# Kernel tuning notes

Measured on AMD Instinct MI355X. Metric: run time of the kernel, lower is better.

The kernel has to match this reference:

```python
import jax, jax.numpy as jnp
import numpy as np

B, S, D, H = 4096, 200, 128, 64


def setup_inputs() -> dict:
    key = jax.random.key(0)
    ks = jax.random.split(key, 8)
    X_series = jax.random.normal(ks[0], (B, S, D), dtype=jnp.float32)
    pos_series = jax.random.normal(ks[1], (S, D), dtype=jnp.float32)
    X_item = jax.random.normal(ks[2], (B, D), dtype=jnp.float32)
    valid_mask = jax.random.randint(ks[3], (B, S), 0, 2) > 0
    valid_mask = valid_mask.at[:, 0].set(True)  # avoid all-masked rows (NaN softmax)
    glorot = jax.nn.initializers.glorot_uniform()
    Wc = glorot(ks[4], (D, H), jnp.float32)
    Wp = glorot(ks[5], (D, H), jnp.float32)
    We = glorot(ks[6], (D, H), jnp.float32)
    z = jax.random.normal(ks[7], (H,), dtype=jnp.float32) * 0.1
    return {"X_series": X_series, "pos_series": pos_series, "X_item": X_item,
            "valid_mask": valid_mask, "Wc": Wc, "Wp": Wp, "We": We, "z": z}


def reference(X_series, pos_series, X_item, valid_mask, Wc, Wp, We, z):
    # additive attention pre-activation: [B,S,H]
    pre = (X_item @ Wc)[:, None, :] + X_series @ We + (pos_series @ Wp)[None, :, :]
    # scores: sum over hidden of z * tanh(pre) -> [B,S]
    scores = jnp.einsum('bsh,h->bs', jnp.tanh(pre), z)
    # raw masked score sum (pre-softmax), [B,1]
    score_sum = jnp.sum(jnp.where(valid_mask, scores, 0.0), axis=-1, keepdims=True)
    # masked softmax over seq
    attn = jax.nn.softmax(jnp.where(valid_mask, scores, -jnp.inf), axis=-1)
    # weighted sum over seq -> [B,D]
    attention_output = jnp.einsum('bs,bsd->bd', attn, X_series)
    return jnp.concatenate([attention_output, score_sum], axis=1)
```

## Files before the change

kernel.cpp:

```cpp
#include <hip/hip_runtime.h>

#define BB 4096
#define SS 200
#define DD 128
#define HH 64
#define NT 13
#define OUTW (DD + 1)

typedef __attribute__((ext_vector_type(4))) float f32x4;
typedef _Float16 f16x8 __attribute__((ext_vector_type(8)));

template <int CTRL>
__device__ __forceinline__ float dpp_add(float x) {
  int xi = __float_as_int(x);
  int yi = __builtin_amdgcn_update_dpp(xi, xi, CTRL, 0xF, 0xF, false);
  return x + __int_as_float(yi);
}
__device__ __forceinline__ float row16_sum(float x) {
  x = dpp_add<0xB1>(x);
  x = dpp_add<0x4E>(x);
  x = dpp_add<0x124>(x);
  x = dpp_add<0x128>(x);
  return x;
}

__global__ void setup_kernel(const float* __restrict__ pos,
                             const float* __restrict__ Wp,
                             const float* __restrict__ We,
                             const void* __restrict__ maskv,
                             float* __restrict__ Pmat,
                             _Float16* __restrict__ Bfrag,
                             int* __restrict__ flag) {
  __shared__ int anyf[4];
  const int blk = blockIdx.x;
  const int t = threadIdx.x;
  if (blk < SS) {
    if (t < HH) {
      float acc = 0.f;
      #pragma unroll 8
      for (int d = 0; d < DD; ++d) acc = fmaf(pos[blk * DD + d], Wp[d * HH + t], acc);
      Pmat[blk * HH + t] = acc;
    }
  } else if (blk == SS) {
    for (int id = t; id < 1024; id += 256) {
      int lane = id & 63;
      int kt = (id >> 6) & 3;
      int ct = id >> 8;
      int kbase = kt * 32 + 8 * (lane >> 4);
      int n = ct * 16 + (lane & 15);
      _Float16* dst = Bfrag + id * 8;
      #pragma unroll
      for (int j = 0; j < 8; ++j) dst[j] = (_Float16)We[(kbase + j) * HH + n];
    }
  } else {
    const unsigned char* mb = (const unsigned char*)maskv;
    int local = 0;
    for (int i = t; i < 4096; i += 256)
      if ((i & 3) != 0 && mb[i] != 0) local = 1;
    unsigned long long bal = __ballot(local != 0);
    if ((t & 63) == 0) anyf[t >> 6] = (bal != 0ull) ? 1 : 0;
    __syncthreads();
    if (t == 0) *flag = (anyf[0] | anyf[1] | anyf[2] | anyf[3]);
  }
}

__global__ void swizzle_kernel(const float* __restrict__ Pmat, _Float16* __restrict__ Psw) {
  const int tile = blockIdx.x;
  const int tid = threadIdx.x;
  const int half = tid >> 6, lane = tid & 63;
  _Float16* dst = Psw + ((size_t)(tile * 2 + half) * 64 + lane) * 8;
  #pragma unroll
  for (int e = 0; e < 8; ++e) {
    const int ct = (half << 1) | (e >> 2);
    const int r = e & 3;
    int s = tile * 16 + ((lane >> 4) << 2) + r;
    if (s >= SS) s = SS - 1;
    dst[e] = (_Float16)Pmat[s * HH + ct * 16 + (lane & 15)];
  }
}

__global__ __launch_bounds__(512, 2) void fused_kernel(
    const float* __restrict__ Xs, const float* __restrict__ Xi,
    const void* __restrict__ maskv, const float* __restrict__ Wc,
    const float* __restrict__ zv,
    const _Float16* __restrict__ Comb,
    const int* __restrict__ flagp,
    float* __restrict__ out) {
  __shared__ __align__(16) _Float16 bf_lds[8192];
  __shared__ __align__(16) float xlds[8][2][2048];

  const int t = threadIdx.x;
  const int lane = t & 63;
  const int w = t >> 6;
  const int lg = lane >> 4;
  const int lr = lane & 15;
  const int b = blockIdx.x * 8 + w;

  const float* Xrow = Xs + (size_t)b * (SS * DD);
  const f16x8* pswb = (const f16x8*)(Comb + 8192);

  auto stage_tile = [&](int tt, int buf) {
    float* dst = &xlds[w][buf][0];
    #pragma unroll
    for (int k = 0; k < 8; ++k) {
      const int row = 2 * k + (lane >> 5);
      int grow = tt * 16 + row; if (grow >= SS) grow = SS - 1;
      const int c = (lane & 31) ^ row;
      const float* src = Xrow + (size_t)grow * DD + c * 4;
      __builtin_amdgcn_global_load_lds(
          (const __attribute__((address_space(1))) void*)src,
          (__attribute__((address_space(3))) void*)(dst + k * 256),
          16, 0, 0);
    }
  };

  stage_tile(0, 0);
  f16x8 pn0 = pswb[lane];
  f16x8 pn1 = pswb[64 + lane];

  {
    const f32x4* src = (const f32x4*)Comb;
    f32x4* dst = (f32x4*)bf_lds;
    dst[t] = src[t];
    dst[t + 512] = src[t + 512];
  }

  float c = 0.f;
  {
    const float* xi = Xi + (size_t)b * DD;
    const float* wc = Wc + lane;
    #pragma unroll 8
    for (int d = 0; d < DD; ++d) c = fmaf(xi[d], wc[d * HH], c);
  }

  const int mflag = *flagp;
  unsigned mbits = 0;
  if (mflag) {
    const unsigned char* mbp = (const unsigned char*)maskv + (size_t)b * SS;
    #pragma unroll
    for (int tt = 0; tt < NT; ++tt) {
      const int srow = tt * 16 + lr;
      unsigned v = (srow < SS) ? (unsigned)mbp[srow] : 0u;
      mbits |= (v ? 1u : 0u) << tt;
    }
  } else {
    const int* mip = (const int*)maskv + (size_t)b * SS;
    #pragma unroll
    for (int tt = 0; tt < NT; ++tt) {
      const int srow = tt * 16 + lr;
      unsigned v = (srow < SS) ? (unsigned)(mip[srow] != 0) : 0u;
      mbits |= v << tt;
    }
  }

  float c4[4], z4[4];
  {
    const float zl = zv[lane];
    #pragma unroll
    for (int ct = 0; ct < 4; ++ct) {
      c4[ct] = __shfl(c, ct * 16 + lr, 64);
      z4[ct] = __shfl(zl, ct * 16 + lr, 64);
    }
  }
  __syncthreads();

  const f16x8* bp = (const f16x8*)bf_lds;
  float part[4][8];
  #pragma unroll
  for (int kt = 0; kt < 4; ++kt)
    #pragma unroll
    for (int j = 0; j < 8; ++j) part[kt][j] = 0.f;
  float usum = 0.f, ssum = 0.f;
  int cur = 0;

  for (int tt = 0; tt < NT; ++tt) {
    asm volatile("s_waitcnt vmcnt(0)" ::: "memory");
    __builtin_amdgcn_sched_barrier(0);
    f32x4 acc[4];
    #pragma unroll
    for (int ct = 0; ct < 4; ++ct) {
      #pragma unroll
      for (int r = 0; r < 4; ++r) {
        const float pv = (ct < 2) ? (float)pn0[ct * 4 + r] : (float)pn1[(ct - 2) * 4 + r];
        acc[ct][r] = pv + c4[ct];
      }
    }
    if (tt + 1 < NT) {
      stage_tile(tt + 1, cur ^ 1);
      pn0 = pswb[(tt + 1) * 128 + lane];
      pn1 = pswb[(tt + 1) * 128 + 64 + lane];
    }
    const float* bufp = &xlds[w][cur][0];
    f16x8 af[4];
    #pragma unroll
    for (int kt = 0; kt < 4; ++kt) {
      const int ch = lg * 2 + kt * 8;
      const f32x4 v0 = *(const f32x4*)&bufp[lr * 128 + (((ch    ) ^ lr) * 4)];
      const f32x4 v1 = *(const f32x4*)&bufp[lr * 128 + (((ch + 1) ^ lr) * 4)];
      f16x8 v;
      v[0] = (_Float16)v0[0]; v[1] = (_Float16)v0[1];
      v[2] = (_Float16)v0[2]; v[3] = (_Float16)v0[3];
      v[4] = (_Float16)v1[0]; v[5] = (_Float16)v1[1];
      v[6] = (_Float16)v1[2]; v[7] = (_Float16)v1[3];
      af[kt] = v;
    }
    #pragma unroll
    for (int kt = 0; kt < 4; ++kt)
      #pragma unroll
      for (int ct = 0; ct < 4; ++ct)
        acc[ct] = __builtin_amdgcn_mfma_f32_16x16x32_f16(af[kt], bp[(ct * 4 + kt) * 64 + lane],
                                                         acc[ct], 0, 0, 0);
    float sc[4];
    #pragma unroll
    for (int r = 0; r < 4; ++r) {
      float p = 0.f;
      #pragma unroll
      for (int ct = 0; ct < 4; ++ct) {
        const float e2 = __expf(2.f * acc[ct][r]);
        const float th = 1.f - 2.f * __builtin_amdgcn_rcpf(e2 + 1.f);
        p = fmaf(z4[ct], th, p);
      }
      sc[r] = row16_sum(p);
    }
    const float s01 = (lr & 1) ? sc[1] : sc[0];
    const float s23 = (lr & 1) ? sc[3] : sc[2];
    const float sel = (lr & 2) ? s23 : s01;
    const float mysc = __shfl(sel, ((lr >> 2) << 4) | lr, 64);
    const bool mv = (mbits >> tt) & 1u;
    const float u = mv ? __expf(mysc) : 0.f;
    ssum += mv ? mysc : 0.f;
    usum += u;
    #pragma unroll
    for (int kt = 0; kt < 4; ++kt)
      #pragma unroll
      for (int j = 0; j < 8; ++j)
        part[kt][j] = fmaf(u, (float)af[kt][j], part[kt][j]);
    cur ^= 1;
  }

  #pragma unroll
  for (int kt = 0; kt < 4; ++kt)
    #pragma unroll
    for (int j = 0; j < 8; ++j)
      part[kt][j] = row16_sum(part[kt][j]);
  usum = row16_sum(usum);
  ssum = row16_sum(ssum);

  const float inv = 1.f / usum;
  if (lr == 0) {
    float* ob = out + (size_t)b * OUTW;
    #pragma unroll
    for (int kt = 0; kt < 4; ++kt)
      #pragma unroll
      for (int j = 0; j < 8; ++j)
        ob[kt * 32 + lg * 8 + j] = part[kt][j] * inv;
  }
  if (lane == 8) out[(size_t)b * OUTW + DD] = ssum;
}

extern "C" void kernel_launch(void* const* d_in, const int* in_sizes, int n_in,
                              void* d_out, int out_size, void* d_ws, size_t ws_size,
                              hipStream_t stream) {
  const float* Xs  = (const float*)d_in[0];
  const float* pos = (const float*)d_in[1];
  const float* Xi  = (const float*)d_in[2];
  const void*  mk  = d_in[3];
  const float* Wc  = (const float*)d_in[4];
  const float* Wp  = (const float*)d_in[5];
  const float* We  = (const float*)d_in[6];
  const float* zv  = (const float*)d_in[7];
  float* out = (float*)d_out;

  char* ws = (char*)d_ws;
  int*      flag  = (int*)ws;
  float*    Pmat  = (float*)(ws + 256);
  _Float16* Bfrag = (_Float16*)(ws + 256 + SS * HH * 4);
  _Float16* Psw   = (_Float16*)(ws + 256 + SS * HH * 4 + 16384);

  setup_kernel<<<SS + 2, 256, 0, stream>>>(pos, Wp, We, mk, Pmat, Bfrag, flag);
  swizzle_kernel<<<NT, 128, 0, stream>>>(Pmat, Psw);
  fused_kernel<<<BB / 8, 512, 0, stream>>>(Xs, Xi, mk, Wc, zv, Bfrag, flag, out);
}
```

Baseline: 106.5 us.

## Prefetch two tiles ahead and hold MFMA B operands in registers

The X-tile staging pipeline goes from one tile ahead to two tiles ahead. The loop is unrolled by two with a partial vmcnt wait, and each buffer is refilled only after its LDS reads have drained. The combined weight fragments move from shared memory into 16 per-lane registers, which removes the LDS copy, the block barrier and the per-MFMA LDS loads. The cost is higher register pressure under launch_bounds(512,2) and reliance on hand-counted vmcnt values.

```diff
diff --git a/kernel.cpp b/kernel.cpp
--- a/kernel.cpp
+++ b/kernel.cpp
@@ -86,7 +86,6 @@
     const _Float16* __restrict__ Comb,
     const int* __restrict__ flagp,
     float* __restrict__ out) {
-  __shared__ __align__(16) _Float16 bf_lds[8192];
   __shared__ __align__(16) float xlds[8][2][2048];
 
   const int t = threadIdx.x;
@@ -114,15 +113,16 @@
     }
   };
 
+  f16x8 pnA0 = pswb[lane],       pnA1 = pswb[64 + lane];
   stage_tile(0, 0);
-  f16x8 pn0 = pswb[lane];
-  f16x8 pn1 = pswb[64 + lane];
-
+  f16x8 pnB0 = pswb[128 + lane], pnB1 = pswb[192 + lane];
+  stage_tile(1, 1);
+
+  f16x8 bfr[16];
   {
-    const f32x4* src = (const f32x4*)Comb;
-    f32x4* dst = (f32x4*)bf_lds;
-    dst[t] = src[t];
-    dst[t + 512] = src[t + 512];
+    const f16x8* bg = (const f16x8*)Comb;
+    #pragma unroll
+    for (int i = 0; i < 16; ++i) bfr[i] = bg[i * 64 + lane];
   }
 
   float c = 0.f;
@@ -162,54 +162,57 @@
       z4[ct] = __shfl(zl, ct * 16 + lr, 64);
     }
   }
-  __syncthreads();
-
-  const f16x8* bp = (const f16x8*)bf_lds;
+
   float part[4][8];
   #pragma unroll
   for (int kt = 0; kt < 4; ++kt)
     #pragma unroll
     for (int j = 0; j < 8; ++j) part[kt][j] = 0.f;
   float usum = 0.f, ssum = 0.f;
-  int cur = 0;
-
-  for (int tt = 0; tt < NT; ++tt) {
-    asm volatile("s_waitcnt vmcnt(0)" ::: "memory");
+
+  auto body = [&](int tt, f16x8& p0, f16x8& p1, int bufIdx, bool last) {
+    if (last) { asm volatile("s_waitcnt vmcnt(0)" ::: "memory"); }
+    else      { asm volatile("s_waitcnt vmcnt(10)" ::: "memory"); }
     __builtin_amdgcn_sched_barrier(0);
     f32x4 acc[4];
     #pragma unroll
     for (int ct = 0; ct < 4; ++ct) {
       #pragma unroll
       for (int r = 0; r < 4; ++r) {
-        const float pv = (ct < 2) ? (float)pn0[ct * 4 + r] : (float)pn1[(ct - 2) * 4 + r];
+        const float pv = (ct < 2) ? (float)p0[ct * 4 + r] : (float)p1[(ct - 2) * 4 + r];
         acc[ct][r] = pv + c4[ct];
       }
     }
-    if (tt + 1 < NT) {
-      stage_tile(tt + 1, cur ^ 1);
-      pn0 = pswb[(tt + 1) * 128 + lane];
-      pn1 = pswb[(tt + 1) * 128 + 64 + lane];
-    }
-    const float* bufp = &xlds[w][cur][0];
-    f16x8 af[4];
+    const float* bufp = &xlds[w][bufIdx][0];
+    f32x4 v0[4], v1[4];
     #pragma unroll
     for (int kt = 0; kt < 4; ++kt) {
       const int ch = lg * 2 + kt * 8;
-      const f32x4 v0 = *(const f32x4*)&bufp[lr * 128 + (((ch    ) ^ lr) * 4)];
-      const f32x4 v1 = *(const f32x4*)&bufp[lr * 128 + (((ch + 1) ^ lr) * 4)];
+      v0[kt] = *(const f32x4*)&bufp[lr * 128 + (((ch    ) ^ lr) * 4)];
+      v1[kt] = *(const f32x4*)&bufp[lr * 128 + (((ch + 1) ^ lr) * 4)];
+    }
+    asm volatile("s_waitcnt lgkmcnt(0)" ::: "memory");
+    __builtin_amdgcn_sched_barrier(0);
+    if (tt + 2 < NT) {
+      p0 = pswb[(tt + 2) * 128 + lane];
+      p1 = pswb[(tt + 2) * 128 + 64 + lane];
+      stage_tile(tt + 2, bufIdx);
+    }
+    f16x8 af[4];
+    #pragma unroll
+    for (int kt = 0; kt < 4; ++kt) {
       f16x8 v;
-      v[0] = (_Float16)v0[0]; v[1] = (_Float16)v0[1];
-      v[2] = (_Float16)v0[2]; v[3] = (_Float16)v0[3];
-      v[4] = (_Float16)v1[0]; v[5] = (_Float16)v1[1];
-      v[6] = (_Float16)v1[2]; v[7] = (_Float16)v1[3];
+      v[0] = (_Float16)v0[kt][0]; v[1] = (_Float16)v0[kt][1];
+      v[2] = (_Float16)v0[kt][2]; v[3] = (_Float16)v0[kt][3];
+      v[4] = (_Float16)v1[kt][0]; v[5] = (_Float16)v1[kt][1];
+      v[6] = (_Float16)v1[kt][2]; v[7] = (_Float16)v1[kt][3];
       af[kt] = v;
     }
     #pragma unroll
     for (int kt = 0; kt < 4; ++kt)
       #pragma unroll
       for (int ct = 0; ct < 4; ++ct)
-        acc[ct] = __builtin_amdgcn_mfma_f32_16x16x32_f16(af[kt], bp[(ct * 4 + kt) * 64 + lane],
-                                                         acc[ct], 0, 0, 0);
+        acc[ct] = __builtin_amdgcn_mfma_f32_16x16x32_f16(af[kt], bfr[ct * 4 + kt], acc[ct], 0, 0, 0);
     float sc[4];
     #pragma unroll
     for (int r = 0; r < 4; ++r) {
@@ -235,8 +238,13 @@
       #pragma unroll
       for (int j = 0; j < 8; ++j)
         part[kt][j] = fmaf(u, (float)af[kt][j], part[kt][j]);
-    cur ^= 1;
-  }
+  };
+
+  for (int tt = 0; tt + 1 < NT; tt += 2) {
+    body(tt,     pnA0, pnA1, 0, false);
+    body(tt + 1, pnB0, pnB1, 1, false);
+  }
+  body(NT - 1, pnA0, pnA1, 0, true);
 
   #pragma unroll
   for (int kt = 0; kt < 4; ++kt)
```

Measured after the change: 124.6 us. 17.0% more time.

## Precompute item projection in setup kernel, keep We fragments in registers, shrink blocks

Applied to the files above, without the earlier changes.

Moves the X_item @ Wc projection out of the fused kernel into extra setup-kernel blocks that write a per-batch workspace, so the main kernel only loads four values per lane. The We MFMA B-fragments are now held in 16 registers per lane instead of being staged in shared memory, which removes the LDS copy and the block-wide barrier. Blocks shrink from 8 waves to 4, halving the shared footprint per block. The cost is higher register pressure, which may hurt occupancy, and a larger setup launch.

```diff
diff --git a/kernel.cpp b/kernel.cpp
--- a/kernel.cpp
+++ b/kernel.cpp
@@ -28,8 +28,11 @@
                              const float* __restrict__ Wp,
                              const float* __restrict__ We,
                              const void* __restrict__ maskv,
+                             const float* __restrict__ Xi,
+                             const float* __restrict__ Wc,
                              float* __restrict__ Pmat,
                              _Float16* __restrict__ Bfrag,
+                             float* __restrict__ cw,
                              int* __restrict__ flag) {
   __shared__ int anyf[4];
   const int blk = blockIdx.x;
@@ -52,7 +55,7 @@
       #pragma unroll
       for (int j = 0; j < 8; ++j) dst[j] = (_Float16)We[(kbase + j) * HH + n];
     }
-  } else {
+  } else if (blk == SS + 1) {
     const unsigned char* mb = (const unsigned char*)maskv;
     int local = 0;
     for (int i = t; i < 4096; i += 256)
@@ -61,6 +64,21 @@
     if ((t & 63) == 0) anyf[t >> 6] = (bal != 0ull) ? 1 : 0;
     __syncthreads();
     if (t == 0) *flag = (anyf[0] | anyf[1] | anyf[2] | anyf[3]);
+  } else {
+    const int w = t >> 6, lane = t & 63;
+    const int base = (blk - (SS + 2)) * 8 + w * 2;
+    const float* xi0 = Xi + (size_t)base * DD;
+    const float* xi1 = xi0 + DD;
+    const float* wc = Wc + lane;
+    float a0 = 0.f, a1 = 0.f;
+    #pragma unroll 8
+    for (int d = 0; d < DD; ++d) {
+      const float wv = wc[d * HH];
+      a0 = fmaf(xi0[d], wv, a0);
+      a1 = fmaf(xi1[d], wv, a1);
+    }
+    cw[(size_t)base * HH + lane] = a0;
+    cw[(size_t)(base + 1) * HH + lane] = a1;
   }
 }
 
@@ -79,22 +97,20 @@
   }
 }
 
-__global__ __launch_bounds__(512, 2) void fused_kernel(
-    const float* __restrict__ Xs, const float* __restrict__ Xi,
-    const void* __restrict__ maskv, const float* __restrict__ Wc,
-    const float* __restrict__ zv,
+__global__ __launch_bounds__(256, 2) void fused_kernel(
+    const float* __restrict__ Xs, const void* __restrict__ maskv,
+    const float* __restrict__ zv, const float* __restrict__ cw,
     const _Float16* __restrict__ Comb,
     const int* __restrict__ flagp,
     float* __restrict__ out) {
-  __shared__ __align__(16) _Float16 bf_lds[8192];
-  __shared__ __align__(16) float xlds[8][2][2048];
+  __shared__ __align__(16) float xlds[4][2][2048];
 
   const int t = threadIdx.x;
   const int lane = t & 63;
   const int w = t >> 6;
   const int lg = lane >> 4;
   const int lr = lane & 15;
-  const int b = blockIdx.x * 8 + w;
+  const int b = blockIdx.x * 4 + w;
 
   const float* Xrow = Xs + (size_t)b * (SS * DD);
   const f16x8* pswb = (const f16x8*)(Comb + 8192);
@@ -118,19 +134,18 @@
   f16x8 pn0 = pswb[lane];
   f16x8 pn1 = pswb[64 + lane];
 
+  f16x8 bfr[16];
   {
-    const f32x4* src = (const f32x4*)Comb;
-    f32x4* dst = (f32x4*)bf_lds;
-    dst[t] = src[t];
-    dst[t + 512] = src[t + 512];
-  }
-
-  float c = 0.f;
-  {
-    const float* xi = Xi + (size_t)b * DD;
-    const float* wc = Wc + lane;
-    #pragma unroll 8
-    for (int d = 0; d < DD; ++d) c = fmaf(xi[d], wc[d * HH], c);
+    const f16x8* bg = (const f16x8*)Comb;
+    #pragma unroll
+    for (int i = 0; i < 16; ++i) bfr[i] = bg[i * 64 + lane];
+  }
+
+  float c4[4], z4[4];
+  #pragma unroll
+  for (int ct = 0; ct < 4; ++ct) {
+    c4[ct] = cw[(size_t)b * HH + ct * 16 + lr];
+    z4[ct] = zv[ct * 16 + lr];
   }
 
   const int mflag = *flagp;
@@ -153,18 +168,6 @@
     }
   }
 
-  float c4[4], z4[4];
-  {
-    const float zl = zv[lane];
-    #pragma unroll
-    for (int ct = 0; ct < 4; ++ct) {
-      c4[ct] = __shfl(c, ct * 16 + lr, 64);
-      z4[ct] = __shfl(zl, ct * 16 + lr, 64);
-    }
-  }
-  __syncthreads();
-
-  const f16x8* bp = (const f16x8*)bf_lds;
   float part[4][8];
   #pragma unroll
   for (int kt = 0; kt < 4; ++kt)
@@ -208,8 +211,7 @@
     for (int kt = 0; kt < 4; ++kt)
       #pragma unroll
       for (int ct = 0; ct < 4; ++ct)
-        acc[ct] = __builtin_amdgcn_mfma_f32_16x16x32_f16(af[kt], bp[(ct * 4 + kt) * 64 + lane],
-                                                         acc[ct], 0, 0, 0);
+        acc[ct] = __builtin_amdgcn_mfma_f32_16x16x32_f16(af[kt], bfr[ct * 4 + kt], acc[ct], 0, 0, 0);
     float sc[4];
     #pragma unroll
     for (int r = 0; r < 4; ++r) {
@@ -276,8 +278,10 @@
   float*    Pmat  = (float*)(ws + 256);
   _Float16* Bfrag = (_Float16*)(ws + 256 + SS * HH * 4);
   _Float16* Psw   = (_Float16*)(ws + 256 + SS * HH * 4 + 16384);
-
-  setup_kernel<<<SS + 2, 256, 0, stream>>>(pos, Wp, We, mk, Pmat, Bfrag, flag);
+  float*    cw    = (float*)(ws + 94464);
+
+  setup_kernel<<<SS + 2 + BB / 8, 256, 0, stream>>>(pos, Wp, We, mk, Xi, Wc,
+                                                    Pmat, Bfrag, cw, flag);
   swizzle_kernel<<<NT, 128, 0, stream>>>(Pmat, Psw);
-  fused_kernel<<<BB / 8, 512, 0, stream>>>(Xs, Xi, mk, Wc, zv, Bfrag, flag, out);
-}
+  fused_kernel<<<BB / 4, 256, 0, stream>>>(Xs, mk, zv, cw, Bfrag, flag, out);
+}
```

Measured after the change: 95.44 us. -10.4%, faster.
